# Kernel tuning notes

Hardware: AMD Instinct MI355X
Metric: run time of the kernel (lower is better)

The kernel has to match this reference:

```python
import jax, jax.numpy as jnp
import numpy as np

# Module config: point_dim=2, channels_in=16, channels_out=16, mlp_channels=[8,8], use_bias=False
# set_quad(24) -> N=24 Gauss-Legendre points per axis, decay_param=(24/4)**4
# set_output_locs(12) -> 12x12=144 output locations
N_QUAD = 24
M_SIDE = 12
CI = 16
CO = 16
HID = 8
PDIM = 2
BATCH = 32
DECAY = (N_QUAD / 4.0) ** 4  # 1296.0


def setup_inputs() -> dict:
    key = jax.random.key(0)
    ks = jax.random.split(key, 4)
    # Gauss-Legendre quadrature (glpair equivalent)
    qn, qw = np.polynomial.legendre.leggauss(N_QUAD)
    quad_nodes = jnp.asarray(qn, jnp.float32)
    quad_weights = jnp.asarray(qw, jnp.float32)
    # set_output_locs(M_SIDE): meshgrid('xy') of M_SIDE Gauss nodes, row k=i*m+j -> (n_j, n_i)
    on, _ = np.polynomial.legendre.leggauss(M_SIDE)
    on = jnp.asarray(on, jnp.float32)
    output_locs = jnp.stack([jnp.tile(on, M_SIDE), jnp.repeat(on, M_SIDE)], axis=-1)  # (144, 2)
    features = jax.random.normal(ks[0], (BATCH, CI, N_QUAD * N_QUAD), jnp.float32)
    # One Sin-MLP (2->8->8->1, no bias) per (out,in) channel pair; torch Linear init U(-1/sqrt(fan_in), +)
    def lin(k, fi, fo):
        b = 1.0 / np.sqrt(fi)
        return jax.random.uniform(k, (CO, CI, fi, fo), jnp.float32, -b, b)
    W1 = lin(ks[1], PDIM, HID)
    W2 = lin(ks[2], HID, HID)
    W3 = lin(ks[3], HID, 1)
    return dict(features=features, output_locs=output_locs, quad_nodes=quad_nodes,
                quad_weights=quad_weights, W1=W1, W2=W2, W3=W3)


def _forward(features, output_locs, quad_nodes, quad_weights, W1, W2, W3):
    n = quad_nodes.shape[0]
    # rquad(level=2) flattened: feature index k = i*n + j maps to node (n_j, n_i), weight w_i*w_j
    nodes2d = jnp.stack([jnp.tile(quad_nodes, n), jnp.repeat(quad_nodes, n)], axis=-1)  # (K, 2)
    w2d = jnp.repeat(quad_weights, n) * jnp.tile(quad_weights, n)                      # (K,)
    x = output_locs[:, None, :] - nodes2d[None, :, :]   # (M, K, 2) kernel eval offsets
    M, K, _ = x.shape
    xf = x.reshape(M * K, PDIM)                          # (P, 2), P = M*K
    # eval_MLPs: grouped tiny MLPs over all (out,in) pairs, Sin activations
    h = jnp.sin(jnp.einsum('pd,ocdh->ocph', xf, W1))     # (CO, CI, P, HID)
    h = jnp.sin(jnp.einsum('ocph,ochg->ocpg', h, W2))    # (CO, CI, P, HID)
    w = jnp.einsum('ocpg,ocg->ocp', h, W3[..., 0])       # (CO, CI, P)
    # bump: e * exp(-1/(1 - decay*||x||^4)) inside compact support, 0 outside
    da = DECAY * jnp.sum(xf * xf, axis=-1) ** 2          # decay * ||x||^4, (P,)
    inside = da < 1.0
    den = jnp.where(inside, 1.0 - da, 1.0)
    bump = jnp.where(inside, jnp.float32(np.e) * jnp.exp(-1.0 / den), 0.0)
    mesh_w = jnp.tile(w2d, M)                            # per p = m*K + k -> w2d[k]
    kern = (w * bump * mesh_w).reshape(CO, CI, M, K)
    # quadrature contraction over input channels and quadrature points
    return jnp.einsum('ocmk,bck->bom', kern, features)   # (B, CO, M)


def reference(features, output_locs, quad_nodes, quad_weights, W1, W2, W3):
    return _forward(features, output_locs, quad_nodes, quad_weights, W1, W2, W3)
```

## Files before the change

kernel.cpp:

```cpp
#include <hip/hip_runtime.h>
#include <math.h>


#define NQ 24
#define M_TOT 144
#define NB 32

__device__ __forceinline__ float sin_poly(float x) {
    float z = x * x;
    float r = fmaf(z, 2.7557313707070068e-06f, -1.9841269659586510e-04f);
    r = fmaf(z, r, 8.3333333332248946e-03f);
    r = fmaf(z, r, -1.6666666666666632e-01f);
    return fmaf(x * z, r, x);
}

__global__ __launch_bounds__(256, 2)
void quadconv_kernel(const float* __restrict__ F,
                     const float* __restrict__ OL,
                     const float* __restrict__ QN,
                     const float* __restrict__ QW,
                     const float* __restrict__ W1,
                     const float* __restrict__ W2,
                     const float* __restrict__ W3,
                     float* __restrict__ OUT) {
    const int ik = blockIdx.x;
    const int m  = blockIdx.y;
    const int t  = threadIdx.x;
    const int o  = t >> 4;
    const int c  = t & 15;

    const float oy = OL[2 * m + 1];
    const float x1 = oy - QN[ik];
    const float x1sq = x1 * x1;
    if (x1sq >= 1.0f / 36.0f) return;

    const float ox   = OL[2 * m];
    const float qwik = QW[ik];

    __shared__ float f_s[NQ * 512];
    __shared__ float qn_s[NQ], qw_s[NQ];

    if (t < NQ) { qn_s[t] = QN[t]; qw_s[t] = QW[t]; }

    float w1r[16], w2r[64], w3r[8];
    {
        const float4* p1 = (const float4*)(W1 + t * 16);
        #pragma unroll
        for (int i = 0; i < 4; ++i) ((float4*)w1r)[i] = p1[i];
        const float4* p2 = (const float4*)(W2 + t * 64);
        #pragma unroll
        for (int i = 0; i < 16; ++i) ((float4*)w2r)[i] = p2[i];
        const float4* p3 = (const float4*)(W3 + t * 8);
        #pragma unroll
        for (int i = 0; i < 2; ++i) ((float4*)w3r)[i] = p3[i];
    }

    {
        const int kbase = ik * NQ;
        #pragma unroll
        for (int pp = 0; pp < 2; ++pp) {
            const int p  = t + pp * 256;
            const int b  = p >> 4;
            const int cc = p & 15;
            const float4* src = (const float4*)(F + b * 9216 + cc * 576 + kbase);
            float4 q[6];
            #pragma unroll
            for (int j = 0; j < 6; ++j) q[j] = src[j];
            const float* qs = (const float*)q;
            #pragma unroll
            for (int j = 0; j < NQ; ++j) f_s[j * 512 + p] = qs[j];
        }
    }
    __syncthreads();

    float acc[NB];
    #pragma unroll
    for (int b = 0; b < NB; ++b) acc[b] = 0.0f;
    bool any = false;

    for (int jk = 0; jk < NQ; ++jk) {
        float x0 = ox - qn_s[jk];
        float r2 = fmaf(x0, x0, x1sq);
        float da = 1296.0f * r2 * r2;
        if (da >= 1.0f) continue;
        any = true;

        float bump = 2.718281828459045f * expf(-1.0f / (1.0f - da));
        float kscale = bump * qwik * qw_s[jk];

        float h1[8];
        #pragma unroll
        for (int h = 0; h < 8; ++h)
            h1[h] = sin_poly(fmaf(x0, w1r[h], x1 * w1r[8 + h]));

        float wsum = 0.0f;
        #pragma unroll
        for (int g = 0; g < 8; ++g) {
            float z = h1[0] * w2r[g];
            #pragma unroll
            for (int h = 1; h < 8; ++h)
                z = fmaf(h1[h], w2r[h * 8 + g], z);
            wsum = fmaf(sin_poly(z), w3r[g], wsum);
        }

        float kv = wsum * kscale;
        const float* fp = &f_s[jk * 512 + c];
        #pragma unroll
        for (int b = 0; b < NB; ++b)
            acc[b] = fmaf(kv, fp[b * 16], acc[b]);
    }

    if (!any) return;

    #pragma unroll
    for (int b = 0; b < NB; ++b) {
        float v = acc[b];
        v += __shfl_xor(v, 1);
        v += __shfl_xor(v, 2);
        v += __shfl_xor(v, 4);
        v += __shfl_xor(v, 8);
        acc[b] = v;
    }
    if (c == 0) {
        #pragma unroll
        for (int b = 0; b < NB; ++b)
            atomicAdd(&OUT[b * (16 * M_TOT) + o * M_TOT + m], acc[b]);
    }
}

extern "C" void kernel_launch(void* const* d_in, const int* in_sizes, int n_in,
                              void* d_out, int out_size, void* d_ws, size_t ws_size,
                              hipStream_t stream) {
    const float* F  = (const float*)d_in[0];
    const float* OL = (const float*)d_in[1];
    const float* QN = (const float*)d_in[2];
    const float* QW = (const float*)d_in[3];
    const float* W1 = (const float*)d_in[4];
    const float* W2 = (const float*)d_in[5];
    const float* W3 = (const float*)d_in[6];
    float* OUT = (float*)d_out;
    hipMemsetAsync(d_out, 0, (size_t)out_size * sizeof(float), stream);
    quadconv_kernel<<<dim3(NQ, M_TOT), dim3(256), 0, stream>>>(F, OL, QN, QW, W1, W2, W3, OUT);
}
```

Baseline: 95.31 us.

## Launch only support-intersecting quadrature rows and load a narrow column window

The grid shrinks from 24 blocks per output location to 8 slots. Each block scans the quadrature nodes to find the row it is responsible for, then exits if that row lies outside the bump support. For the chosen row it finds the column range inside the support and loads only an 8-wide window of features instead of all 24 columns. It computes up to 6 kernel values in registers before the contraction, which is now fully unrolled, and the feature global loads overlap with the MLP evaluation. This assumes at most 8 rows and 6 columns fall within the support for the fixed decay and node set.

Result: no change. 96.04 us (+0.8%).

```diff
diff --git a/kernel.cpp b/kernel.cpp
--- a/kernel.cpp
+++ b/kernel.cpp
@@ -5,6 +5,8 @@
 #define NQ 24
 #define M_TOT 144
 #define NB 32
+#define SLOTS 8
+#define R2MAX (1.0f / 36.0f)
 
 __device__ __forceinline__ float sin_poly(float x) {
     float z = x * x;
@@ -23,24 +25,46 @@
                      const float* __restrict__ W2,
                      const float* __restrict__ W3,
                      float* __restrict__ OUT) {
-    const int ik = blockIdx.x;
-    const int m  = blockIdx.y;
-    const int t  = threadIdx.x;
-    const int o  = t >> 4;
-    const int c  = t & 15;
+    const int slot = blockIdx.x;
+    const int m    = blockIdx.y;
+    const int t    = threadIdx.x;
+    const int c    = t & 15;
+    const int o    = t >> 4;
 
+    const float ox = OL[2 * m];
     const float oy = OL[2 * m + 1];
+
+    int ik = -1, cnt = 0;
+    for (int i = 0; i < NQ; ++i) {
+        float d = oy - QN[i];
+        if (d * d < R2MAX) { if (cnt == slot) ik = i; ++cnt; }
+    }
+    if (ik < 0) return;
     const float x1 = oy - QN[ik];
     const float x1sq = x1 * x1;
-    if (x1sq >= 1.0f / 36.0f) return;
 
-    const float ox   = OL[2 * m];
-    const float qwik = QW[ik];
+    const float lim = R2MAX - x1sq;
+    int jk0 = NQ, jk1 = -1;
+    for (int j = 0; j < NQ; ++j) {
+        float d = ox - QN[j];
+        if (d * d < lim) { if (jk1 < 0) jk0 = j; jk1 = j; }
+    }
+    if (jk1 < 0) return;
+    jk0 = min(jk0, 18);
+    const int w0   = min(jk0 & ~1, 16);
+    const int joff = jk0 - w0;
 
-    __shared__ float f_s[NQ * 512];
-    __shared__ float qn_s[NQ], qw_s[NQ];
+    __shared__ float f_s[8 * 512];
 
-    if (t < NQ) { qn_s[t] = QN[t]; qw_s[t] = QW[t]; }
+    const int kbase = ik * NQ + w0;
+    float2 q[8];
+    {
+        const float* base = F + (t >> 4) * 9216 + (t & 15) * 576 + kbase;
+        const float2* s0 = (const float2*)base;
+        const float2* s1 = (const float2*)(base + 16 * 9216);
+        #pragma unroll
+        for (int i = 0; i < 4; ++i) { q[i] = s0[i]; q[i + 4] = s1[i]; }
+    }
 
     float w1r[16], w2r[64], w3r[8];
     {
@@ -55,62 +79,55 @@
         for (int i = 0; i < 2; ++i) ((float4*)w3r)[i] = p3[i];
     }
 
-    {
-        const int kbase = ik * NQ;
-        #pragma unroll
-        for (int pp = 0; pp < 2; ++pp) {
-            const int p  = t + pp * 256;
-            const int b  = p >> 4;
-            const int cc = p & 15;
-            const float4* src = (const float4*)(F + b * 9216 + cc * 576 + kbase);
-            float4 q[6];
+    const float qwik = QW[ik];
+    float kvr[6];
+    #pragma unroll
+    for (int j = 0; j < 6; ++j) {
+        const int jk = jk0 + j;
+        const float x0 = ox - QN[jk];
+        const float r2 = fmaf(x0, x0, x1sq);
+        const float da = 1296.0f * r2 * r2;
+        float kv = 0.0f;
+        if (da < 1.0f) {
+            const float kscale =
+                2.718281828459045f * __expf(-1.0f / (1.0f - da)) * qwik * QW[jk];
+            float h1[8];
             #pragma unroll
-            for (int j = 0; j < 6; ++j) q[j] = src[j];
-            const float* qs = (const float*)q;
+            for (int h = 0; h < 8; ++h)
+                h1[h] = sin_poly(fmaf(x0, w1r[h], x1 * w1r[8 + h]));
+            float wsum = 0.0f;
             #pragma unroll
-            for (int j = 0; j < NQ; ++j) f_s[j * 512 + p] = qs[j];
+            for (int g = 0; g < 8; ++g) {
+                float z = h1[0] * w2r[g];
+                #pragma unroll
+                for (int h = 1; h < 8; ++h)
+                    z = fmaf(h1[h], w2r[h * 8 + g], z);
+                wsum = fmaf(sin_poly(z), w3r[g], wsum);
+            }
+            kv = wsum * kscale;
         }
+        kvr[j] = kv;
+    }
+
+    #pragma unroll
+    for (int i = 0; i < 4; ++i) {
+        f_s[(2 * i) * 512 + t]           = q[i].x;
+        f_s[(2 * i + 1) * 512 + t]       = q[i].y;
+        f_s[(2 * i) * 512 + t + 256]     = q[i + 4].x;
+        f_s[(2 * i + 1) * 512 + t + 256] = q[i + 4].y;
     }
     __syncthreads();
 
     float acc[NB];
+    const float* fp = f_s + joff * 512 + c;
     #pragma unroll
-    for (int b = 0; b < NB; ++b) acc[b] = 0.0f;
-    bool any = false;
-
-    for (int jk = 0; jk < NQ; ++jk) {
-        float x0 = ox - qn_s[jk];
-        float r2 = fmaf(x0, x0, x1sq);
-        float da = 1296.0f * r2 * r2;
-        if (da >= 1.0f) continue;
-        any = true;
-
-        float bump = 2.718281828459045f * expf(-1.0f / (1.0f - da));
-        float kscale = bump * qwik * qw_s[jk];
-
-        float h1[8];
+    for (int b = 0; b < NB; ++b) {
+        float a = 0.0f;
         #pragma unroll
-        for (int h = 0; h < 8; ++h)
-            h1[h] = sin_poly(fmaf(x0, w1r[h], x1 * w1r[8 + h]));
-
-        float wsum = 0.0f;
-        #pragma unroll
-        for (int g = 0; g < 8; ++g) {
-            float z = h1[0] * w2r[g];
-            #pragma unroll
-            for (int h = 1; h < 8; ++h)
-                z = fmaf(h1[h], w2r[h * 8 + g], z);
-            wsum = fmaf(sin_poly(z), w3r[g], wsum);
-        }
-
-        float kv = wsum * kscale;
-        const float* fp = &f_s[jk * 512 + c];
-        #pragma unroll
-        for (int b = 0; b < NB; ++b)
-            acc[b] = fmaf(kv, fp[b * 16], acc[b]);
+        for (int j = 0; j < 6; ++j)
+            a = fmaf(kvr[j], fp[j * 512 + b * 16], a);
+        acc[b] = a;
     }
-
-    if (!any) return;
 
     #pragma unroll
     for (int b = 0; b < NB; ++b) {
@@ -140,5 +157,5 @@
     const float* W3 = (const float*)d_in[6];
     float* OUT = (float*)d_out;
     hipMemsetAsync(d_out, 0, (size_t)out_size * sizeof(float), stream);
-    quadconv_kernel<<<dim3(NQ, M_TOT), dim3(256), 0, stream>>>(F, OL, QN, QW, W1, W2, W3, OUT);
+    quadconv_kernel<<<dim3(SLOTS, M_TOT), dim3(256), 0, stream>>>(F, OL, QN, QW, W1, W2, W3, OUT);
 }
```
